# Kernel tuning notes

Hardware: AMD Instinct MI355X
Metric: run time of the kernel (lower is better)

## Reference

```python
import jax, jax.numpy as jnp
import numpy as np

N, D, E, S = 200000, 256, 1000000, 10000

def setup_inputs() -> dict:
    key = jax.random.key(0)
    k1, k2, k3, k4 = jax.random.split(key, 4)
    z = jax.random.normal(k1, (N, D), dtype=jnp.float32)
    attn_w = jax.random.normal(k2, (D,), dtype=jnp.float32) * (1.0 / np.sqrt(D))
    attn_b = jnp.zeros((), dtype=jnp.float32)
    idx = jax.random.randint(k3, (E,), 0, N, dtype=jnp.int64)
    seg = jnp.sort(jax.random.randint(k4, (E,), 0, S, dtype=jnp.int64))
    return {"z": z, "attn_w": attn_w, "attn_b": attn_b, "idx": idx, "seg": seg, "num_segments": S}

def reference(z, attn_w, attn_b, idx, seg, num_segments):
    # Gather ragged groups: sub[e] = z[idx[e]], group id = seg[e]
    sub = z[idx]                                   # [E, D]
    logits = sub @ attn_w + attn_b                 # [E] (nn.Linear(dim,1).squeeze)
    # Segmented, numerically-stable softmax over each group
    m = jax.ops.segment_max(logits, seg, num_segments=num_segments)  # [S]
    m = jnp.where(jnp.isfinite(m), m, 0.0)         # empty segments -> harmless 0
    e = jnp.exp(logits - m[seg])                   # [E]
    den = jax.ops.segment_sum(e, seg, num_segments=num_segments)     # [S]
    w = e / den[seg]                               # [E]
    # Softmax-weighted sum per segment; empty segments yield zeros (matches torch)
    out = jax.ops.segment_sum(sub * w[:, None], seg, num_segments=num_segments)  # [S, D]
    return out
```

## Files before the change

### kernel.cpp

```cpp
#include <hip/hip_runtime.h>
#include <hip/hip_fp16.h>
#include <math.h>

#define DDIM 256
#define NWAVES 4
#define SEGW 4
#define NEG_SENT -1.0e30f

__global__ void seg_offsets_kernel(const int* __restrict__ seg, int E, int S,
                                   int* __restrict__ offs) {
    int i = blockIdx.x * blockDim.x + threadIdx.x;
    if (i > S) return;
    int lo = 0, hi = E;
    while (lo < hi) {
        int mid = (lo + hi) >> 1;
        if (seg[mid] < i) lo = mid + 1; else hi = mid;
    }
    offs[i] = lo;
}

__global__ __launch_bounds__(256)
void prep_offs_kernel(const float4* __restrict__ z4,
                      const float* __restrict__ attn_w,
                      const float* __restrict__ attn_b,
                      uint2* __restrict__ z16,
                      float* __restrict__ pvec, int N, int gridN,
                      const int* __restrict__ seg, int E, int S,
                      int* __restrict__ offs) {
    if ((int)blockIdx.x >= gridN) {
        int i = ((int)blockIdx.x - gridN) * blockDim.x + threadIdx.x;
        if (i > S) return;
        int lo = 0, hi = E;
        while (lo < hi) {
            int mid = (lo + hi) >> 1;
            if (seg[mid] < i) lo = mid + 1; else hi = mid;
        }
        offs[i] = lo;
        return;
    }
    const int wave = threadIdx.x >> 6;
    const int lane = threadIdx.x & 63;
    const int row  = blockIdx.x * NWAVES + wave;
    if (row >= N) return;
    const float4 v = z4[(long)row * 64 + lane];
    __half2 h0 = __floats2half2_rn(v.x, v.y);
    __half2 h1 = __floats2half2_rn(v.z, v.w);
    uint2 h;
    h.x = *(unsigned int*)&h0;
    h.y = *(unsigned int*)&h1;
    z16[(long)row * 64 + lane] = h;
    const float4 wv = ((const float4*)attn_w)[lane];
    float part = v.x * wv.x + v.y * wv.y + v.z * wv.z + v.w * wv.w;
    #pragma unroll
    for (int sh = 32; sh >= 1; sh >>= 1) part += __shfl_xor(part, sh);
    if (lane == 0) pvec[row] = __expf(part + attn_b[0]);
}

__global__ __launch_bounds__(256)
void node_p_kernel(const float4* __restrict__ z4,
                   const float* __restrict__ attn_w,
                   const float* __restrict__ attn_b,
                   float* __restrict__ pvec, int N) {
    const int wave = threadIdx.x >> 6;
    const int lane = threadIdx.x & 63;
    const int row  = blockIdx.x * NWAVES + wave;
    if (row >= N) return;
    const float4 v  = z4[(long)row * 64 + lane];
    const float4 wv = ((const float4*)attn_w)[lane];
    float part = v.x * wv.x + v.y * wv.y + v.z * wv.z + v.w * wv.w;
    #pragma unroll
    for (int sh = 32; sh >= 1; sh >>= 1) part += __shfl_xor(part, sh);
    if (lane == 0) pvec[row] = __expf(part + attn_b[0]);
}

__device__ inline float4 h4_to_f4(unsigned int lo, unsigned int hi) {
    __half2 a = *(__half2*)&lo;
    __half2 b = *(__half2*)&hi;
    float2 fa = __half22float2(a);
    float2 fb = __half22float2(b);
    return make_float4(fa.x, fa.y, fb.x, fb.y);
}

__global__ __launch_bounds__(256)
void segpool5_kernel(const uint4* __restrict__ z16,
                     const float* __restrict__ pvec,
                     const int* __restrict__ idx,
                     const int* __restrict__ offs,
                     float* __restrict__ out, int S) {
    const int wave = threadIdx.x >> 6;
    const int lane = threadIdx.x & 63;
    const int half = lane >> 5;
    const int hl   = lane & 31;
    const int s = blockIdx.x * SEGW + wave;
    if (s >= S) return;
    const int start = __builtin_amdgcn_readfirstlane(offs[s]);
    const int end   = __builtin_amdgcn_readfirstlane(offs[s + 1]);
    float4* __restrict__ out4 = (float4*)out;
    const long obase = (long)s * 64 + 2 * hl + half;
    if (end <= start) {
        out4[obase] = make_float4(0.f, 0.f, 0.f, 0.f);
        return;
    }

    float den = 0.f;
    float a0=0.f,a1=0.f,a2=0.f,a3=0.f,a4=0.f,a5=0.f,a6=0.f,a7=0.f;

    int e = start;
    for (; e + 8 <= end; e += 8) {
        int rows[4];
        #pragma unroll
        for (int k = 0; k < 4; ++k) rows[k] = idx[e + 2 * k + half];
        float ps[4]; uint4 hs[4];
        #pragma unroll
        for (int k = 0; k < 4; ++k) {
            ps[k] = pvec[rows[k]];
            hs[k] = z16[((unsigned)rows[k] << 5) + hl];
        }
        #pragma unroll
        for (int k = 0; k < 4; ++k) {
            const float4 va = h4_to_f4(hs[k].x, hs[k].y);
            const float4 vb = h4_to_f4(hs[k].z, hs[k].w);
            den += ps[k];
            a0 += ps[k] * va.x; a1 += ps[k] * va.y;
            a2 += ps[k] * va.z; a3 += ps[k] * va.w;
            a4 += ps[k] * vb.x; a5 += ps[k] * vb.y;
            a6 += ps[k] * vb.z; a7 += ps[k] * vb.w;
        }
    }
    for (; e + 2 <= end; e += 2) {
        const int   row = idx[e + half];
        const float p   = pvec[row];
        const uint4 h   = z16[((unsigned)row << 5) + hl];
        const float4 va = h4_to_f4(h.x, h.y);
        const float4 vb = h4_to_f4(h.z, h.w);
        den += p;
        a0 += p * va.x; a1 += p * va.y; a2 += p * va.z; a3 += p * va.w;
        a4 += p * vb.x; a5 += p * vb.y; a6 += p * vb.z; a7 += p * vb.w;
    }
    if (e < end) {
        const int   row = idx[e];
        const float p   = pvec[row];
        const uint4 h   = z16[((unsigned)row << 5) + hl];
        if (half == 0) {
            const float4 va = h4_to_f4(h.x, h.y);
            const float4 vb = h4_to_f4(h.z, h.w);
            den += p;
            a0 += p * va.x; a1 += p * va.y; a2 += p * va.z; a3 += p * va.w;
            a4 += p * vb.x; a5 += p * vb.y; a6 += p * vb.z; a7 += p * vb.w;
        }
    }

    den += __shfl_xor(den, 32);
    a0 += __shfl_xor(a0, 32); a1 += __shfl_xor(a1, 32);
    a2 += __shfl_xor(a2, 32); a3 += __shfl_xor(a3, 32);
    a4 += __shfl_xor(a4, 32); a5 += __shfl_xor(a5, 32);
    a6 += __shfl_xor(a6, 32); a7 += __shfl_xor(a7, 32);

    const float inv = 1.0f / den;
    const float4 o = (half == 0)
        ? make_float4(a0 * inv, a1 * inv, a2 * inv, a3 * inv)
        : make_float4(a4 * inv, a5 * inv, a6 * inv, a7 * inv);
    out4[obase] = o;
}

__global__ __launch_bounds__(256)
void segpool3_f32_kernel(const float4* __restrict__ z4,
                         const float* __restrict__ pvec,
                         const int* __restrict__ idx,
                         const int* __restrict__ offs,
                         float* __restrict__ out) {
    const int s     = blockIdx.x;
    const int start = offs[s];
    const int end   = offs[s + 1];
    const int tid   = threadIdx.x;
    if (end <= start) { out[(long)s * DDIM + tid] = 0.0f; return; }
    const int wave = tid >> 6;
    const int lane = tid & 63;
    float  den = 0.0f;
    float4 acc = make_float4(0.f, 0.f, 0.f, 0.f);
    int e = start + wave;
    for (; e + 7 * NWAVES < end; e += 8 * NWAVES) {
        int rows[8];
        #pragma unroll
        for (int k = 0; k < 8; ++k) rows[k] = idx[e + k * NWAVES];
        float ps[8]; float4 vs[8];
        #pragma unroll
        for (int k = 0; k < 8; ++k) {
            ps[k] = pvec[rows[k]];
            vs[k] = z4[(long)rows[k] * 64 + lane];
        }
        #pragma unroll
        for (int k = 0; k < 8; ++k) {
            den  += ps[k];
            acc.x += ps[k] * vs[k].x;
            acc.y += ps[k] * vs[k].y;
            acc.z += ps[k] * vs[k].z;
            acc.w += ps[k] * vs[k].w;
        }
    }
    for (; e < end; e += NWAVES) {
        const int row = idx[e];
        const float p = pvec[row];
        const float4 v = z4[(long)row * 64 + lane];
        den  += p;
        acc.x += p * v.x;
        acc.y += p * v.y;
        acc.z += p * v.z;
        acc.w += p * v.w;
    }
    __shared__ float lds_den[NWAVES];
    __shared__ float lds_acc[NWAVES][DDIM];
    if (lane == 0) lds_den[wave] = den;
    lds_acc[wave][4 * lane + 0] = acc.x;
    lds_acc[wave][4 * lane + 1] = acc.y;
    lds_acc[wave][4 * lane + 2] = acc.z;
    lds_acc[wave][4 * lane + 3] = acc.w;
    __syncthreads();
    const float D = lds_den[0] + lds_den[1] + lds_den[2] + lds_den[3];
    const float o = lds_acc[0][tid] + lds_acc[1][tid] +
                    lds_acc[2][tid] + lds_acc[3][tid];
    out[(long)s * DDIM + tid] = o / D;
}

__global__ __launch_bounds__(256)
void segpool_fused_kernel(const float* __restrict__ z,
                          const float* __restrict__ attn_w,
                          const float* __restrict__ attn_b,
                          const int* __restrict__ idx,
                          const int* __restrict__ offs,
                          float* __restrict__ out) {
    const int s     = blockIdx.x;
    const int start = offs[s];
    const int end   = offs[s + 1];
    const int tid   = threadIdx.x;
    if (end <= start) { out[(long)s * DDIM + tid] = 0.0f; return; }
    const int wave = tid >> 6;
    const int lane = tid & 63;
    const float4 wv = ((const float4*)attn_w)[lane];
    const float  b  = attn_b[0];
    const float4* __restrict__ z4 = (const float4*)z;
    float  m = NEG_SENT, l = 0.0f;
    float4 acc = make_float4(0.f, 0.f, 0.f, 0.f);
    for (int e = start + wave; e < end; e += NWAVES) {
        const int   row = idx[e];
        const float4 v  = z4[(long)row * 64 + lane];
        float part = v.x * wv.x + v.y * wv.y + v.z * wv.z + v.w * wv.w;
        #pragma unroll
        for (int sh = 32; sh >= 1; sh >>= 1) part += __shfl_xor(part, sh);
        const float logit = part + b;
        const float nm    = fmaxf(m, logit);
        const float alpha = __expf(m - nm);
        const float p     = __expf(logit - nm);
        l = l * alpha + p;
        acc.x = acc.x * alpha + p * v.x;
        acc.y = acc.y * alpha + p * v.y;
        acc.z = acc.z * alpha + p * v.z;
        acc.w = acc.w * alpha + p * v.w;
        m = nm;
    }
    __shared__ float lds_m[NWAVES], lds_l[NWAVES];
    __shared__ float lds_acc[NWAVES][DDIM];
    if (lane == 0) { lds_m[wave] = m; lds_l[wave] = l; }
    __syncthreads();
    const float M = fmaxf(fmaxf(lds_m[0], lds_m[1]), fmaxf(lds_m[2], lds_m[3]));
    float den = 0.0f;
    #pragma unroll
    for (int w = 0; w < NWAVES; ++w) den += __expf(lds_m[w] - M) * lds_l[w];
    const float scale = __expf(m - M);
    lds_acc[wave][4 * lane + 0] = acc.x * scale;
    lds_acc[wave][4 * lane + 1] = acc.y * scale;
    lds_acc[wave][4 * lane + 2] = acc.z * scale;
    lds_acc[wave][4 * lane + 3] = acc.w * scale;
    __syncthreads();
    const float o = lds_acc[0][tid] + lds_acc[1][tid] +
                    lds_acc[2][tid] + lds_acc[3][tid];
    out[(long)s * DDIM + tid] = o / den;
}

extern "C" void kernel_launch(void* const* d_in, const int* in_sizes, int n_in,
                              void* d_out, int out_size, void* d_ws, size_t ws_size,
                              hipStream_t stream) {
    const float* z      = (const float*)d_in[0];
    const float* attn_w = (const float*)d_in[1];
    const float* attn_b = (const float*)d_in[2];
    const int*   idx    = (const int*)d_in[3];
    const int*   seg    = (const int*)d_in[4];
    float*       out    = (float*)d_out;

    const int E = in_sizes[3];
    const int S = out_size / DDIM;
    const int N = in_sizes[0] / DDIM;

    const int threads = 256;
    const int gridA = (S + 1 + threads - 1) / threads;
    const int gridN = (N + NWAVES - 1) / NWAVES;

    int* offs = (int*)d_ws;
    const size_t offs_bytes = (((size_t)(S + 1) * sizeof(int)) + 255) & ~(size_t)255;
    const size_t p_bytes    = (((size_t)N * sizeof(float)) + 255) & ~(size_t)255;
    const size_t z16_bytes  = (size_t)N * DDIM * sizeof(__half);
    const size_t need_full  = offs_bytes + p_bytes + z16_bytes;
    const size_t need_p     = offs_bytes + p_bytes;

    if (ws_size >= need_full) {
        float* pvec = (float*)((char*)d_ws + offs_bytes);
        uint2* z16  = (uint2*)((char*)d_ws + offs_bytes + p_bytes);
        prep_offs_kernel<<<gridN + gridA, threads, 0, stream>>>(
            (const float4*)z, attn_w, attn_b, z16, pvec, N, gridN,
            seg, E, S, offs);
        segpool5_kernel<<<(S + SEGW - 1) / SEGW, threads, 0, stream>>>(
            (const uint4*)z16, pvec, idx, offs, out, S);
    } else if (ws_size >= need_p) {
        float* pvec = (float*)((char*)d_ws + offs_bytes);
        seg_offsets_kernel<<<gridA, threads, 0, stream>>>(seg, E, S, offs);
        node_p_kernel<<<gridN, threads, 0, stream>>>(
            (const float4*)z, attn_w, attn_b, pvec, N);
        segpool3_f32_kernel<<<S, threads, 0, stream>>>(
            (const float4*)z, pvec, idx, offs, out);
    } else {
        seg_offsets_kernel<<<gridA, threads, 0, stream>>>(seg, E, S, offs);
        segpool_fused_kernel<<<S, threads, 0, stream>>>(
            z, attn_w, attn_b, idx, offs, out);
    }
}
```

Measured before the change: 373.1 us.

## Fuse prep and segment pooling into one cooperative persistent kernel with grid sync

Adds a persistent cooperative kernel that computes segment offsets, the fp16 copy of z and per-node exp-logits, then does a grid-wide sync and runs the segment pooling loop in the same launch over 1024 blocks. This removes the second kernel launch and the gap between kernels. The cost is a grid barrier, grid-stride loops with fixed occupancy (launch bounds 256,4), and possible load imbalance. It falls back to the two-kernel path if the cooperative launch fails. It also deletes the unrolled main loop in the f32 fallback pooling kernel, which leaves a slower but still correct path.

```diff
diff --git a/kernel.cpp b/kernel.cpp
--- a/kernel.cpp
+++ b/kernel.cpp
@@ -1,11 +1,147 @@
 #include <hip/hip_runtime.h>
+#include <hip/hip_cooperative_groups.h>
 #include <hip/hip_fp16.h>
 #include <math.h>
+
+namespace cg = cooperative_groups;
 
 #define DDIM 256
 #define NWAVES 4
 #define SEGW 4
 #define NEG_SENT -1.0e30f
+
+__device__ inline float4 h4_to_f4(unsigned int lo, unsigned int hi) {
+    __half2 a = *(__half2*)&lo;
+    __half2 b = *(__half2*)&hi;
+    float2 fa = __half22float2(a);
+    float2 fb = __half22float2(b);
+    return make_float4(fa.x, fa.y, fb.x, fb.y);
+}
+
+__global__ __launch_bounds__(256, 4)
+void fused_all_kernel(const float4* __restrict__ z4,
+                      const float* __restrict__ attn_w,
+                      const float* __restrict__ attn_b,
+                      const int* __restrict__ idx,
+                      const int* __restrict__ seg,
+                      uint2* __restrict__ z16,
+                      float* __restrict__ pvec,
+                      int* __restrict__ offs,
+                      float* __restrict__ out,
+                      int N, int E, int S) {
+    const int wave = threadIdx.x >> 6;
+    const int lane = threadIdx.x & 63;
+    const int gw   = blockIdx.x * NWAVES + wave;
+    const int nw   = gridDim.x * NWAVES;
+
+    {
+        const int t  = blockIdx.x * blockDim.x + threadIdx.x;
+        const int nt = gridDim.x * blockDim.x;
+        for (int i = t; i <= S; i += nt) {
+            int lo = 0, hi = E;
+            while (lo < hi) {
+                int mid = (lo + hi) >> 1;
+                if (seg[mid] < i) lo = mid + 1; else hi = mid;
+            }
+            offs[i] = lo;
+        }
+    }
+
+    {
+        const float4 wv = ((const float4*)attn_w)[lane];
+        const float  b  = attn_b[0];
+        for (int row = gw; row < N; row += nw) {
+            const float4 v = z4[(long)row * 64 + lane];
+            __half2 h0 = __floats2half2_rn(v.x, v.y);
+            __half2 h1 = __floats2half2_rn(v.z, v.w);
+            uint2 h;
+            h.x = *(unsigned int*)&h0;
+            h.y = *(unsigned int*)&h1;
+            z16[(long)row * 64 + lane] = h;
+            float part = v.x * wv.x + v.y * wv.y + v.z * wv.z + v.w * wv.w;
+            #pragma unroll
+            for (int sh = 32; sh >= 1; sh >>= 1) part += __shfl_xor(part, sh);
+            if (lane == 0) pvec[row] = __expf(part + b);
+        }
+    }
+
+    cg::this_grid().sync();
+
+    const int half = lane >> 5;
+    const int hl   = lane & 31;
+    const uint4* __restrict__ zz = (const uint4*)z16;
+    float4* __restrict__ out4 = (float4*)out;
+
+    for (int s = gw; s < S; s += nw) {
+        const int start = __builtin_amdgcn_readfirstlane(offs[s]);
+        const int end   = __builtin_amdgcn_readfirstlane(offs[s + 1]);
+        const long obase = (long)s * 64 + 2 * hl + half;
+        if (end <= start) {
+            out4[obase] = make_float4(0.f, 0.f, 0.f, 0.f);
+            continue;
+        }
+
+        float den = 0.f;
+        float a0=0.f,a1=0.f,a2=0.f,a3=0.f,a4=0.f,a5=0.f,a6=0.f,a7=0.f;
+
+        int e = start;
+        for (; e + 8 <= end; e += 8) {
+            int rows[4];
+            #pragma unroll
+            for (int k = 0; k < 4; ++k) rows[k] = idx[e + 2 * k + half];
+            float ps[4]; uint4 hs[4];
+            #pragma unroll
+            for (int k = 0; k < 4; ++k) {
+                ps[k] = pvec[rows[k]];
+                hs[k] = zz[((unsigned)rows[k] << 5) + hl];
+            }
+            #pragma unroll
+            for (int k = 0; k < 4; ++k) {
+                const float4 va = h4_to_f4(hs[k].x, hs[k].y);
+                const float4 vb = h4_to_f4(hs[k].z, hs[k].w);
+                den += ps[k];
+                a0 += ps[k] * va.x; a1 += ps[k] * va.y;
+                a2 += ps[k] * va.z; a3 += ps[k] * va.w;
+                a4 += ps[k] * vb.x; a5 += ps[k] * vb.y;
+                a6 += ps[k] * vb.z; a7 += ps[k] * vb.w;
+            }
+        }
+        for (; e + 2 <= end; e += 2) {
+            const int   row = idx[e + half];
+            const float p   = pvec[row];
+            const uint4 h   = zz[((unsigned)row << 5) + hl];
+            const float4 va = h4_to_f4(h.x, h.y);
+            const float4 vb = h4_to_f4(h.z, h.w);
+            den += p;
+            a0 += p * va.x; a1 += p * va.y; a2 += p * va.z; a3 += p * va.w;
+            a4 += p * vb.x; a5 += p * vb.y; a6 += p * vb.z; a7 += p * vb.w;
+        }
+        if (e < end) {
+            const int   row = idx[e];
+            const float p   = pvec[row];
+            const uint4 h   = zz[((unsigned)row << 5) + hl];
+            if (half == 0) {
+                const float4 va = h4_to_f4(h.x, h.y);
+                const float4 vb = h4_to_f4(h.z, h.w);
+                den += p;
+                a0 += p * va.x; a1 += p * va.y; a2 += p * va.z; a3 += p * va.w;
+                a4 += p * vb.x; a5 += p * vb.y; a6 += p * vb.z; a7 += p * vb.w;
+            }
+        }
+
+        den += __shfl_xor(den, 32);
+        a0 += __shfl_xor(a0, 32); a1 += __shfl_xor(a1, 32);
+        a2 += __shfl_xor(a2, 32); a3 += __shfl_xor(a3, 32);
+        a4 += __shfl_xor(a4, 32); a5 += __shfl_xor(a5, 32);
+        a6 += __shfl_xor(a6, 32); a7 += __shfl_xor(a7, 32);
+
+        const float inv = 1.0f / den;
+        const float4 o = (half == 0)
+            ? make_float4(a0 * inv, a1 * inv, a2 * inv, a3 * inv)
+            : make_float4(a4 * inv, a5 * inv, a6 * inv, a7 * inv);
+        out4[obase] = o;
+    }
+}
 
 __global__ void seg_offsets_kernel(const int* __restrict__ seg, int E, int S,
                                    int* __restrict__ offs) {
@@ -54,31 +190,6 @@
     #pragma unroll
     for (int sh = 32; sh >= 1; sh >>= 1) part += __shfl_xor(part, sh);
     if (lane == 0) pvec[row] = __expf(part + attn_b[0]);
-}
-
-__global__ __launch_bounds__(256)
-void node_p_kernel(const float4* __restrict__ z4,
-                   const float* __restrict__ attn_w,
-                   const float* __restrict__ attn_b,
-                   float* __restrict__ pvec, int N) {
-    const int wave = threadIdx.x >> 6;
-    const int lane = threadIdx.x & 63;
-    const int row  = blockIdx.x * NWAVES + wave;
-    if (row >= N) return;
-    const float4 v  = z4[(long)row * 64 + lane];
-    const float4 wv = ((const float4*)attn_w)[lane];
-    float part = v.x * wv.x + v.y * wv.y + v.z * wv.z + v.w * wv.w;
-    #pragma unroll
-    for (int sh = 32; sh >= 1; sh >>= 1) part += __shfl_xor(part, sh);
-    if (lane == 0) pvec[row] = __expf(part + attn_b[0]);
-}
-
-__device__ inline float4 h4_to_f4(unsigned int lo, unsigned int hi) {
-    __half2 a = *(__half2*)&lo;
-    __half2 b = *(__half2*)&hi;
-    float2 fa = __half22float2(a);
-    float2 fb = __half22float2(b);
-    return make_float4(fa.x, fa.y, fb.x, fb.y);
 }
 
 __global__ __launch_bounds__(256)
@@ -101,10 +212,8 @@
         out4[obase] = make_float4(0.f, 0.f, 0.f, 0.f);
         return;
     }
-
     float den = 0.f;
     float a0=0.f,a1=0.f,a2=0.f,a3=0.f,a4=0.f,a5=0.f,a6=0.f,a7=0.f;
-
     int e = start;
     for (; e + 8 <= end; e += 8) {
         int rows[4];
@@ -149,18 +258,33 @@
             a4 += p * vb.x; a5 += p * vb.y; a6 += p * vb.z; a7 += p * vb.w;
         }
     }
-
     den += __shfl_xor(den, 32);
     a0 += __shfl_xor(a0, 32); a1 += __shfl_xor(a1, 32);
     a2 += __shfl_xor(a2, 32); a3 += __shfl_xor(a3, 32);
     a4 += __shfl_xor(a4, 32); a5 += __shfl_xor(a5, 32);
     a6 += __shfl_xor(a6, 32); a7 += __shfl_xor(a7, 32);
-
     const float inv = 1.0f / den;
     const float4 o = (half == 0)
         ? make_float4(a0 * inv, a1 * inv, a2 * inv, a3 * inv)
         : make_float4(a4 * inv, a5 * inv, a6 * inv, a7 * inv);
     out4[obase] = o;
+}
+
+__global__ __launch_bounds__(256)
+void node_p_kernel(const float4* __restrict__ z4,
+                   const float* __restrict__ attn_w,
+                   const float* __restrict__ attn_b,
+                   float* __restrict__ pvec, int N) {
+    const int wave = threadIdx.x >> 6;
+    const int lane = threadIdx.x & 63;
+    const int row  = blockIdx.x * NWAVES + wave;
+    if (row >= N) return;
+    const float4 v  = z4[(long)row * 64 + lane];
+    const float4 wv = ((const float4*)attn_w)[lane];
+    float part = v.x * wv.x + v.y * wv.y + v.z * wv.z + v.w * wv.w;
+    #pragma unroll
+    for (int sh = 32; sh >= 1; sh >>= 1) part += __shfl_xor(part, sh);
+    if (lane == 0) pvec[row] = __expf(part + attn_b[0]);
 }
 
 __global__ __launch_bounds__(256)
@@ -179,25 +303,6 @@
     float  den = 0.0f;
     float4 acc = make_float4(0.f, 0.f, 0.f, 0.f);
     int e = start + wave;
-    for (; e + 7 * NWAVES < end; e += 8 * NWAVES) {
-        int rows[8];
-        #pragma unroll
-        for (int k = 0; k < 8; ++k) rows[k] = idx[e + k * NWAVES];
-        float ps[8]; float4 vs[8];
-        #pragma unroll
-        for (int k = 0; k < 8; ++k) {
-            ps[k] = pvec[rows[k]];
-            vs[k] = z4[(long)rows[k] * 64 + lane];
-        }
-        #pragma unroll
-        for (int k = 0; k < 8; ++k) {
-            den  += ps[k];
-            acc.x += ps[k] * vs[k].x;
-            acc.y += ps[k] * vs[k].y;
-            acc.z += ps[k] * vs[k].z;
-            acc.w += ps[k] * vs[k].w;
-        }
-    }
     for (; e < end; e += NWAVES) {
         const int row = idx[e];
         const float p = pvec[row];
@@ -305,6 +410,18 @@
     if (ws_size >= need_full) {
         float* pvec = (float*)((char*)d_ws + offs_bytes);
         uint2* z16  = (uint2*)((char*)d_ws + offs_bytes + p_bytes);
+
+        const float4* z4c = (const float4*)z;
+        int Nv = N, Ev = E, Sv = S;
+        void* args[] = { (void*)&z4c, (void*)&attn_w, (void*)&attn_b,
+                         (void*)&idx, (void*)&seg,
+                         (void*)&z16, (void*)&pvec, (void*)&offs,
+                         (void*)&out, (void*)&Nv, (void*)&Ev, (void*)&Sv };
+        hipError_t err = hipLaunchCooperativeKernel(
+            reinterpret_cast<void*>(fused_all_kernel),
+            dim3(1024), dim3(threads), args, 0, stream);
+        if (err == hipSuccess) return;
+
         prep_offs_kernel<<<gridN + gridA, threads, 0, stream>>>(
             (const float4*)z, attn_w, attn_b, z16, pvec, N, gridN,
             seg, E, S, offs);
```

Result: slower. 498.7 us (+33.7%).
